# Performance work log

Hardware: AMD Instinct MI355X
Metric: run time of the kernel (lower is better)

The kernel has to match this reference:

```python
import jax, jax.numpy as jnp
import numpy as np

NQ = 4
PI_HALF = np.pi / 2
HAD = jnp.array([[1, 1], [1, -1]], dtype=jnp.complex64) / np.sqrt(2)
CNOT = jnp.array([[1, 0, 0, 0], [0, 1, 0, 0], [0, 0, 0, 1], [0, 0, 1, 0]], dtype=jnp.complex64)
_bits = (np.arange(2 ** NQ)[:, None] >> np.arange(NQ - 1, -1, -1)[None, :]) & 1
ZSIGNS = jnp.asarray(1.0 - 2.0 * _bits, jnp.float32)  # [16, NQ]


def _ry(theta):
    c = jnp.cos(theta / 2).astype(jnp.complex64)
    s = jnp.sin(theta / 2).astype(jnp.complex64)
    return jnp.stack([jnp.stack([c, -s], -1), jnp.stack([s, c], -1)], -2)  # [...,2,2]


def _rot(phi, theta, omega):
    # PennyLane Rot = RZ(omega) @ RY(theta) @ RZ(phi)
    c = jnp.cos(theta / 2).astype(jnp.complex64)
    s = jnp.sin(theta / 2).astype(jnp.complex64)
    ep = jnp.exp(0.5j * phi).astype(jnp.complex64)
    eo = jnp.exp(0.5j * omega).astype(jnp.complex64)
    return jnp.stack([jnp.stack([jnp.conj(ep) * jnp.conj(eo) * c, -ep * jnp.conj(eo) * s]),
                      jnp.stack([jnp.conj(ep) * eo * s, ep * eo * c])])


def _cry(theta):
    # controlled-RY, batched: [B] -> [B,4,4], basis order (control, target)
    B = theta.shape[0]
    U = jnp.zeros((B, 4, 4), jnp.complex64).at[:, 0, 0].set(1.0).at[:, 1, 1].set(1.0)
    return U.at[:, 2:, 2:].set(_ry(theta))


def _apply1(state, U, wire):
    s = jnp.moveaxis(state, wire + 1, 1)
    shp = s.shape
    s = s.reshape(shp[0], 2, -1)
    s = jnp.einsum('ij,bjk->bik', U, s) if U.ndim == 2 else jnp.einsum('bij,bjk->bik', U, s)
    return jnp.moveaxis(s.reshape(shp), 1, wire + 1)


def _apply2(state, U, q0, q1):
    s = jnp.moveaxis(state, (q0 + 1, q1 + 1), (1, 2))
    shp = s.shape
    s = s.reshape(shp[0], 4, -1)
    s = jnp.einsum('ij,bjk->bik', U, s) if U.ndim == 2 else jnp.einsum('bij,bjk->bik', U, s)
    return jnp.moveaxis(s.reshape(shp), (1, 2), (q0 + 1, q1 + 1))


def _init_state(B):
    s = jnp.zeros((B, 2 ** NQ), jnp.complex64).at[:, 0].set(1.0)
    return s.reshape((B,) + (2,) * NQ)


def _zexp(state):
    p = state.reshape(state.shape[0], -1)
    p = p.real ** 2 + p.imag ** 2
    return p @ ZSIGNS  # [B, NQ]


def _attention_circuit(q, k, params):
    # q, k: [E, NQ] angles; params: [NQ, 3] shared
    s = _init_state(q.shape[0])
    for i in range(NQ):
        s = _apply1(s, _ry(q[:, i]), i)
    for i in range(NQ):
        s = _apply1(s, HAD, i)
    for i in range(NQ):
        s = _apply2(s, _cry(k[:, i]), i, (i + 1) % NQ)
    for i in range(NQ):
        s = _apply1(s, _rot(params[i, 0], params[i, 1], params[i, 2]), i)
    return _zexp(s)


def _entangle_circuit(x, params):
    # x: [N, NQ] angles; params: [n_layers, NQ, 3]
    s = _init_state(x.shape[0])
    for i in range(NQ):
        s = _apply1(s, _ry(x[:, i]), i)
    for l in range(params.shape[0]):
        for i in range(NQ - 1):
            s = _apply2(s, CNOT, i, i + 1)
        for i in range(NQ):
            s = _apply1(s, _rot(params[l, i, 0], params[l, i, 1], params[l, i, 2]), i)
        s = _apply2(s, CNOT, 0, NQ - 1)  # n_qubits >= 4
    return _zexp(s)


def _path_circuit(x, params):
    # x: [N, NQ]; params: [3, NQ, 3]
    s = _init_state(x.shape[0])
    for i in range(NQ):
        s = _apply1(s, HAD, i)
    for i in range(NQ):
        s = _apply1(s, _ry(x[:, i]), i)
    for l in range(3):
        for i in range(NQ):
            s = _apply1(s, _rot(params[l, i, 0], params[l, i, 1], params[l, i, 2]), i)
        for i in range(NQ - 1):
            s = _apply2(s, CNOT, i, i + 1)
    return _zexp(s)


def _forward(x, W_in, b_in, lin_W, lin_b, qproj_W, qproj_b, ent_params,
             attq_W, attq_b, attk_W, attk_b, att_qp, path_params,
             path_in_W, path_in_b, path_out_W, path_out_b, out_W, out_b, edge_index):
    N = x.shape[0]
    loops = jnp.arange(N, dtype=edge_index.dtype)
    ei = jnp.concatenate([edge_index, jnp.stack([loops, loops])], axis=1)  # add_self_loops
    src, dst = ei[0], ei[1]
    h = jax.nn.relu(x @ W_in.T + b_in)
    for l in range(lin_W.shape[0]):
        x_cls = h @ lin_W[l].T + lin_b[l]
        xq = _entangle_circuit(jnp.tanh(h[:, :NQ]) * PI_HALF, ent_params[l])
        x_comb = x_cls + xq @ qproj_W[l].T + qproj_b[l]
        q = jnp.tanh(h @ attq_W[l].T + attq_b[l]) * PI_HALF
        k = jnp.tanh(h @ attk_W[l].T + attk_b[l]) * PI_HALF
        scores = _attention_circuit(q[src], k[dst], att_qp[l]).mean(axis=1)  # [E]
        att = jax.nn.softmax(scores)  # global softmax over all edges (faithful)
        h = jax.ops.segment_sum(att[:, None] * x_comb[src], dst, num_segments=N)
        h = jax.nn.relu(h)  # dropout is identity at eval
    pq = jnp.tanh(h @ path_in_W.T + path_in_b) * PI_HALF
    h = _path_circuit(pq, path_params) @ path_out_W.T + path_out_b
    return h @ out_W.T + out_b


def setup_inputs() -> dict:
    key = jax.random.key(0)
    ks = jax.random.split(key, 22)
    N, E, D_in, D_h, D_out, L = 20000, 300000, 64, 128, 32, 2
    w = lambda k, shape: jax.random.normal(k, shape, jnp.float32) * 0.1
    return {
        'x': jax.random.normal(ks[0], (N, D_in), jnp.float32),
        'W_in': w(ks[1], (D_h, D_in)), 'b_in': w(ks[2], (D_h,)),
        'lin_W': w(ks[3], (L, D_h, D_h)), 'lin_b': w(ks[4], (L, D_h)),
        'qproj_W': w(ks[5], (L, D_h, NQ)), 'qproj_b': w(ks[6], (L, D_h)),
        'ent_params': w(ks[7], (L, 2, NQ, 3)),
        'attq_W': w(ks[8], (L, NQ, D_h)), 'attq_b': w(ks[9], (L, NQ)),
        'attk_W': w(ks[10], (L, NQ, D_h)), 'attk_b': w(ks[11], (L, NQ)),
        'att_qp': w(ks[12], (L, NQ, 3)),
        'path_params': w(ks[13], (3, NQ, 3)),
        'path_in_W': w(ks[14], (NQ, D_h)), 'path_in_b': w(ks[15], (NQ,)),
        'path_out_W': w(ks[16], (D_h, NQ)), 'path_out_b': w(ks[17], (D_h,)),
        'out_W': w(ks[18], (D_out, D_h)), 'out_b': w(ks[19], (D_out,)),
        'edge_index': jax.random.randint(ks[20], (2, E), 0, N, dtype=jnp.int32),
    }


def reference(x, W_in, b_in, lin_W, lin_b, qproj_W, qproj_b, ent_params,
              attq_W, attq_b, attk_W, attk_b, att_qp, path_params,
              path_in_W, path_in_b, path_out_W, path_out_b, out_W, out_b, edge_index):
    return _forward(x, W_in, b_in, lin_W, lin_b, qproj_W, qproj_b, ent_params,
                    attq_W, attq_b, attk_W, attk_b, att_qp, path_params,
                    path_in_W, path_in_b, path_out_W, path_out_b, out_W, out_b, edge_index)
```

## Files before the change

### kernel.cpp

```cpp
#include <hip/hip_runtime.h>
#include <math.h>

#define PI_HALF 1.57079632679489662f

__device__ __forceinline__ float fast_tanh(float x) {
    float e = __expf(2.f * x);
    return 1.f - 2.f * __builtin_amdgcn_rcpf(e + 1.f);
}


__device__ __forceinline__ void prod_init(float sr[16],
        float c0, float s0, float c1, float s1,
        float c2, float s2, float c3, float s3) {
    float p2[4];
    p2[0] = c0 * c1; p2[1] = c0 * s1; p2[2] = s0 * c1; p2[3] = s0 * s1;
    float p3[8];
#pragma unroll
    for (int j = 0; j < 4; ++j) { p3[2 * j] = p2[j] * c2; p3[2 * j + 1] = p2[j] * s2; }
#pragma unroll
    for (int j = 0; j < 8; ++j) { sr[2 * j] = p3[j] * c3; sr[2 * j + 1] = p3[j] * s3; }
}

template<int M>
__device__ __forceinline__ void had_r(float sr[16]) {
    const float r = 0.70710678118654752f;
#pragma unroll
    for (int i = 0; i < 16; ++i) {
        if (i & M) continue;
        const int j = i | M;
        float ar = sr[i], br = sr[j];
        sr[i] = (ar + br) * r;
        sr[j] = (ar - br) * r;
    }
}

template<int MC, int MT>
__device__ __forceinline__ void cry_r(float sr[16], float c, float s) {
#pragma unroll
    for (int i = 0; i < 16; ++i) {
        if (!(i & MC) || (i & MT)) continue;
        const int j = i | MT;
        float ar = sr[i], br = sr[j];
        sr[i] = c * ar - s * br;
        sr[j] = s * ar + c * br;
    }
}

template<int MC, int MT>
__device__ __forceinline__ void cnot_r(float sr[16]) {
#pragma unroll
    for (int i = 0; i < 16; ++i) {
        if (!(i & MC) || (i & MT)) continue;
        const int j = i | MT;
        float t = sr[i]; sr[i] = sr[j]; sr[j] = t;
    }
}

template<int MC, int MT>
__device__ __forceinline__ void cnot_g(float sr[16], float si[16]) {
#pragma unroll
    for (int i = 0; i < 16; ++i) {
        if (!(i & MC) || (i & MT)) continue;
        const int j = i | MT;
        float tr = sr[i], ti = si[i];
        sr[i] = sr[j]; si[i] = si[j];
        sr[j] = tr;    si[j] = ti;
    }
}

template<int M>
__device__ __forceinline__ void rot_pre(float sr[16], float si[16], const float* __restrict__ u) {
    const float u00r = u[0], u00i = u[1], u01r = u[2], u01i = u[3];
    const float u10r = u[4], u10i = u[5], u11r = u[6], u11i = u[7];
#pragma unroll
    for (int i = 0; i < 16; ++i) {
        if (i & M) continue;
        const int j = i | M;
        float ar = sr[i], ai = si[i], br = sr[j], bi = si[j];
        sr[i] = u00r * ar - u00i * ai + u01r * br - u01i * bi;
        si[i] = u00r * ai + u00i * ar + u01r * bi + u01i * br;
        sr[j] = u10r * ar - u10i * ai + u11r * br - u11i * bi;
        si[j] = u10r * ai + u10i * ar + u11r * bi + u11i * br;
    }
}

template<int M>
__device__ __forceinline__ void rot_first(float sr[16], float si[16], const float* __restrict__ u) {
    const float u00r = u[0], u00i = u[1], u01r = u[2], u01i = u[3];
    const float u10r = u[4], u10i = u[5], u11r = u[6], u11i = u[7];
#pragma unroll
    for (int i = 0; i < 16; ++i) {
        if (i & M) continue;
        const int j = i | M;
        float ar = sr[i], br = sr[j];
        sr[i] = u00r * ar + u01r * br;
        si[i] = u00i * ar + u01i * br;
        sr[j] = u10r * ar + u11r * br;
        si[j] = u10i * ar + u11i * br;
    }
}

__device__ __forceinline__ void zexp_g(const float sr[16], const float si[16], float z[4]) {
    float p[16];
#pragma unroll
    for (int i = 0; i < 16; ++i) p[i] = sr[i] * sr[i] + si[i] * si[i];
    z[0] = z[1] = z[2] = z[3] = 0.f;
#pragma unroll
    for (int i = 0; i < 16; ++i) {
        z[0] += (i & 8) ? -p[i] : p[i];
        z[1] += (i & 4) ? -p[i] : p[i];
        z[2] += (i & 2) ? -p[i] : p[i];
        z[3] += (i & 1) ? -p[i] : p[i];
    }
}


__global__ void k_fsi(const float* __restrict__ entp, const float* __restrict__ attqp,
                      const float* __restrict__ pparm,
                      const float* __restrict__ outW, const float* __restrict__ outb,
                      const float* __restrict__ poW, const float* __restrict__ pob,
                      float* __restrict__ rotbuf, float* __restrict__ M,
                      float* __restrict__ v,
                      const float* __restrict__ x, const float* __restrict__ W,
                      const float* __restrict__ b, float* __restrict__ h,
                      int* __restrict__ cnt, float* __restrict__ sumexp, int N) {
    __shared__ float xs[32 * 64];
    const int bb = blockIdx.x;
    const int tid = threadIdx.x;
    {
        const int gid = bb * 256 + tid;
        const int T = gridDim.x * 256;
        for (int i = gid; i < N; i += T) cnt[i] = 0;
        if (gid < 4) sumexp[gid] = 0.f;
    }
    if (bb == 0) {
        const int t = tid;
        if (t < 36) {
            const float* p;
            if (t < 16)      p = entp  + t * 3;
            else if (t < 24) p = attqp + (t - 16) * 3;
            else             p = pparm + (t - 24) * 3;
            float phi = p[0], theta = p[1], omega = p[2];
            float st, ct; sincosf(0.5f * theta, &st, &ct);
            float sp, cp; sincosf(0.5f * (phi + omega), &sp, &cp);
            float sm, cm; sincosf(0.5f * (phi - omega), &sm, &cm);
            float* u = rotbuf + t * 8;
            u[0] =  ct * cp;  u[1] = -ct * sp;
            u[2] = -st * cm;  u[3] = -st * sm;
            u[4] =  st * cm;  u[5] = -st * sm;
            u[6] =  ct * cp;  u[7] =  ct * sp;
        } else if (t >= 64 && t < 192) {
            int t2 = t - 64;
            int o = t2 >> 2, i = t2 & 3;
            float acc = 0.f;
            for (int j = 0; j < 128; ++j) acc += outW[o * 128 + j] * poW[j * 4 + i];
            M[t2] = acc;
        } else if (t >= 192 && t < 224) {
            int o = t - 192;
            float acc = outb[o];
            for (int j = 0; j < 128; ++j) acc += outW[o * 128 + j] * pob[j];
            v[o] = acc;
        }
        return;
    }
    const int base = (bb - 1) * 32;
    for (int idx = tid; idx < 32 * 64; idx += 256) {
        int n = base + (idx >> 6);
        xs[idx] = (n < N) ? x[(size_t)n * 64 + (idx & 63)] : 0.f;
    }
    __syncthreads();
    const int lane = tid & 63;
    const int wv = tid >> 6;
    const int ch0 = lane, ch1 = lane + 64;
    float acc0[8], acc1[8];
#pragma unroll
    for (int n = 0; n < 8; ++n) { acc0[n] = 0.f; acc1[n] = 0.f; }
    const float4* w04 = (const float4*)(W + ch0 * 64);
    const float4* w14 = (const float4*)(W + ch1 * 64);
    for (int c4 = 0; c4 < 16; ++c4) {
        float4 wa = w04[c4];
        float4 wb = w14[c4];
#pragma unroll
        for (int n = 0; n < 8; ++n) {
            float4 hv = *(const float4*)&xs[(wv * 8 + n) * 64 + c4 * 4];
            acc0[n] += wa.x * hv.x + wa.y * hv.y + wa.z * hv.z + wa.w * hv.w;
            acc1[n] += wb.x * hv.x + wb.y * hv.y + wb.z * hv.z + wb.w * hv.w;
        }
    }
    const float b0 = b[ch0];
    const float b1 = b[ch1];
#pragma unroll
    for (int n = 0; n < 8; ++n) {
        int node = base + wv * 8 + n;
        if (node < N) {
            h[(size_t)node * 128 + ch0] = fmaxf(acc0[n] + b0, 0.f);
            h[(size_t)node * 128 + ch1] = fmaxf(acc1[n] + b1, 0.f);
        }
    }
}

__global__ void k_hist(const int* __restrict__ ei, int* __restrict__ cnt, int E, int EP) {
    int e = blockIdx.x * blockDim.x + threadIdx.x;
    if (e >= EP) return;
    int d_ = (e < E) ? ei[E + e] : e - E;
    atomicAdd(&cnt[d_], 1);
}

__global__ void k_scan(const int* __restrict__ cnt, int* __restrict__ off,
                       int* __restrict__ cur, int N) {
    __shared__ int tot[1024];
    const int t = threadIdx.x;
    const int chunk = (N + 1023) >> 10;
    const int s0 = t * chunk;
    const int s1 = min(s0 + chunk, N);
    int sum = 0;
    for (int i = s0; i < s1; ++i) sum += cnt[i];
    tot[t] = sum;
    __syncthreads();
    for (int d = 1; d < 1024; d <<= 1) {
        int v = (t >= d) ? tot[t - d] : 0;
        __syncthreads();
        tot[t] += v;
        __syncthreads();
    }
    int run = (t == 0) ? 0 : tot[t - 1];
    for (int i = s0; i < s1; ++i) {
        off[i] = run; cur[i] = run;
        run += cnt[i];
    }
}

#define HS_STRIDE 132
__global__ void k_entlin(const float* __restrict__ h, const float* __restrict__ rotE2,
                         const float* __restrict__ linW, const float* __restrict__ linb,
                         const float* __restrict__ qpW, const float* __restrict__ qpb,
                         const float* __restrict__ aqW, const float* __restrict__ aqb,
                         const float* __restrict__ akW, const float* __restrict__ akb,
                         float* __restrict__ xcomb, float* __restrict__ qbuf,
                         float* __restrict__ kbuf, int N,
                         const float* __restrict__ sprev,
                         int eblf, const int* __restrict__ ei,
                         int* __restrict__ cur, int* __restrict__ srcs,
                         int* __restrict__ inv, int E, int EP) {
    __shared__ float hs[16 * HS_STRIDE];
    __shared__ float xqs[16 * 4];
    const int tid = threadIdx.x;
    if (blockIdx.x < eblf) {
        int e = blockIdx.x * 128 + tid;
        if (e < EP) {
            int s_, d_;
            if (e < E) { s_ = ei[e]; d_ = ei[E + e]; } else { s_ = d_ = e - E; }
            int pos = atomicAdd(&cur[d_], 1);
            srcs[pos] = s_;
            inv[e] = pos;
        }
        return;
    }
    const int base = (blockIdx.x - eblf) * 16;
    const float scale = sprev ? __builtin_amdgcn_rcpf(sprev[0]) : 1.0f;
    for (int idx = tid; idx < 16 * 32; idx += 128) {
        int n = idx >> 5, c4 = idx & 31;
        int node = base + n;
        float4 hv = (node < N) ? *(const float4*)&h[(size_t)node * 128 + c4 * 4]
                               : make_float4(0.f, 0.f, 0.f, 0.f);
        hv.x *= scale; hv.y *= scale; hv.z *= scale; hv.w *= scale;
        *(float4*)&hs[n * HS_STRIDE + c4 * 4] = hv;
    }
    __syncthreads();
    if (tid < 64) {
#pragma unroll
        for (int rep = 0; rep < 2; ++rep) {
            const int dt = tid + rep * 64;
            const int nl = dt >> 3;
            const int which = dt & 7;
            const int qi = which & 3;
            const float4* Wp4 = (const float4*)(((which < 4) ? aqW : akW) + qi * 128);
            float dot = (which < 4) ? aqb[qi] : akb[qi];
            for (int c4 = 0; c4 < 32; ++c4) {
                float4 w = Wp4[c4];
                float4 hv = *(const float4*)&hs[nl * HS_STRIDE + c4 * 4];
                dot += w.x * hv.x + w.y * hv.y + w.z * hv.z + w.w * hv.w;
            }
            int node = base + nl;
            if (node < N) {
                float halfang = fast_tanh(dot) * (0.5f * PI_HALF);
                float s, c; __sincosf(halfang, &s, &c);
                float* dst = ((which < 4) ? qbuf : kbuf) + (size_t)node * 8 + qi * 2;
                dst[0] = c; dst[1] = s;
            }
        }
    } else if (tid < 80) {
        const int nl = tid - 64;
        if (base + nl < N) {
            float4 hv = *(const float4*)&hs[nl * HS_STRIDE];
            float c0, s0, c1, s1, c2, s2, c3, s3;
            { float a = fast_tanh(hv.x) * (0.5f * PI_HALF); __sincosf(a, &s0, &c0); }
            { float a = fast_tanh(hv.y) * (0.5f * PI_HALF); __sincosf(a, &s1, &c1); }
            { float a = fast_tanh(hv.z) * (0.5f * PI_HALF); __sincosf(a, &s2, &c2); }
            { float a = fast_tanh(hv.w) * (0.5f * PI_HALF); __sincosf(a, &s3, &c3); }
            float sr[16], si[16];
            prod_init(sr, c0, s0, c1, s1, c2, s2, c3, s3);
            cnot_r<8, 4>(sr); cnot_r<4, 2>(sr); cnot_r<2, 1>(sr);
            rot_first<8>(sr, si, rotE2);
            rot_pre<4>(sr, si, rotE2 + 8);
            rot_pre<2>(sr, si, rotE2 + 16);
            rot_pre<1>(sr, si, rotE2 + 24);
            cnot_g<8, 1>(sr, si);
            cnot_g<8, 4>(sr, si); cnot_g<4, 2>(sr, si); cnot_g<2, 1>(sr, si);
            const float* P = rotE2 + 32;
            rot_pre<8>(sr, si, P);
            rot_pre<4>(sr, si, P + 8);
            rot_pre<2>(sr, si, P + 16);
            rot_pre<1>(sr, si, P + 24);
            cnot_g<8, 1>(sr, si);
            float z[4]; zexp_g(sr, si, z);
            xqs[nl * 4 + 0] = z[0]; xqs[nl * 4 + 1] = z[1];
            xqs[nl * 4 + 2] = z[2]; xqs[nl * 4 + 3] = z[3];
        }
    }
    __syncthreads();
    const int lane = tid & 63;
    const int nh = tid >> 6;
    const int ch0 = lane, ch1 = lane + 64;
    float acc0[8], acc1[8];
#pragma unroll
    for (int n = 0; n < 8; ++n) { acc0[n] = 0.f; acc1[n] = 0.f; }
    const float4* w04 = (const float4*)(linW + ch0 * 128);
    const float4* w14 = (const float4*)(linW + ch1 * 128);
    for (int c4 = 0; c4 < 32; ++c4) {
        float4 wa = w04[c4];
        float4 wb = w14[c4];
#pragma unroll
        for (int n = 0; n < 8; ++n) {
            float4 hv = *(const float4*)&hs[(nh * 8 + n) * HS_STRIDE + c4 * 4];
            acc0[n] += wa.x * hv.x + wa.y * hv.y + wa.z * hv.z + wa.w * hv.w;
            acc1[n] += wb.x * hv.x + wb.y * hv.y + wb.z * hv.z + wb.w * hv.w;
        }
    }
    const float b0 = linb[ch0] + qpb[ch0];
    const float b1 = linb[ch1] + qpb[ch1];
    const float q00 = qpW[ch0 * 4 + 0], q01 = qpW[ch0 * 4 + 1];
    const float q02 = qpW[ch0 * 4 + 2], q03 = qpW[ch0 * 4 + 3];
    const float q10 = qpW[ch1 * 4 + 0], q11 = qpW[ch1 * 4 + 1];
    const float q12 = qpW[ch1 * 4 + 2], q13 = qpW[ch1 * 4 + 3];
#pragma unroll
    for (int n = 0; n < 8; ++n) {
        const int nl = nh * 8 + n;
        const int node = base + nl;
        if (node < N) {
            float x0 = xqs[nl * 4 + 0], x1 = xqs[nl * 4 + 1];
            float x2 = xqs[nl * 4 + 2], x3 = xqs[nl * 4 + 3];
            xcomb[(size_t)node * 128 + ch0] = acc0[n] + b0
                + q00 * x0 + q01 * x1 + q02 * x2 + q03 * x3;
            xcomb[(size_t)node * 128 + ch1] = acc1[n] + b1
                + q10 * x0 + q11 * x1 + q12 * x2 + q13 * x3;
        }
    }
}

__global__ void k_att(const float* __restrict__ qb, const float* __restrict__ kb,
                      const int* __restrict__ ei, const float* __restrict__ RA,
                      const int* __restrict__ inv, float* __restrict__ escore,
                      float* __restrict__ sumexp, int E, int EP) {
    __shared__ float red[4];
    int e = blockIdx.x * blockDim.x + threadIdx.x;
    float ex = 0.f;
    if (e < EP) {
        int s_, d_;
        if (e < E) { s_ = ei[e]; d_ = ei[E + e]; } else { s_ = d_ = e - E; }
        float4 qa = *(const float4*)&qb[(size_t)s_ * 8];
        float4 qc = *(const float4*)&qb[(size_t)s_ * 8 + 4];
        float4 ka = *(const float4*)&kb[(size_t)d_ * 8];
        float4 kc = *(const float4*)&kb[(size_t)d_ * 8 + 4];
        float sr[16], si[16];
        prod_init(sr, qa.x, qa.y, qa.z, qa.w, qc.x, qc.y, qc.z, qc.w);
        had_r<8>(sr); had_r<4>(sr); had_r<2>(sr); had_r<1>(sr);
        cry_r<8, 4>(sr, ka.x, ka.y);
        cry_r<4, 2>(sr, ka.z, ka.w);
        cry_r<2, 1>(sr, kc.x, kc.y);
        cry_r<1, 8>(sr, kc.z, kc.w);
        rot_first<8>(sr, si, RA);
        rot_pre<4>(sr, si, RA + 8);
        rot_pre<2>(sr, si, RA + 16);
        rot_pre<1>(sr, si, RA + 24);
        float p0  = sr[0]  * sr[0]  + si[0]  * si[0];
        float p1  = sr[1]  * sr[1]  + si[1]  * si[1];
        float p2  = sr[2]  * sr[2]  + si[2]  * si[2];
        float p4  = sr[4]  * sr[4]  + si[4]  * si[4];
        float p8  = sr[8]  * sr[8]  + si[8]  * si[8];
        float p7  = sr[7]  * sr[7]  + si[7]  * si[7];
        float p11 = sr[11] * sr[11] + si[11] * si[11];
        float p13 = sr[13] * sr[13] + si[13] * si[13];
        float p14 = sr[14] * sr[14] + si[14] * si[14];
        float p15 = sr[15] * sr[15] + si[15] * si[15];
        float sc = (p0 - p15) + 0.5f * ((p1 + p2 + p4 + p8) - (p7 + p11 + p13 + p14));
        ex = __expf(sc);
        escore[inv[e]] = ex;
    }
    float wsum = ex;
#pragma unroll
    for (int d = 32; d; d >>= 1) wsum += __shfl_xor(wsum, d, 64);
    if ((threadIdx.x & 63) == 0) red[threadIdx.x >> 6] = wsum;
    __syncthreads();
    if (threadIdx.x == 0) atomicAdd(sumexp, red[0] + red[1] + red[2] + red[3]);
}

__global__ void k_gather(const float* __restrict__ xcomb, const int* __restrict__ srcs,
                         const float* __restrict__ escore, const int* __restrict__ off,
                         const int* __restrict__ cnt, float* __restrict__ h) {
    __shared__ int sS[128];
    __shared__ float wS[128];
    const int b = blockIdx.x;
    const int tid = threadIdx.x;
    const int start = off[b];
    const int num = cnt[b];
    float acc = 0.f;
    for (int base = 0; base < num; base += 128) {
        int m = min(128, num - base);
        if (tid < m) {
            sS[tid] = srcs[start + base + tid];
            wS[tid] = escore[start + base + tid];
        }
        __syncthreads();
        int i = 0;
        for (; i + 8 <= m; i += 8) {
            float v0 = xcomb[(size_t)sS[i + 0] * 128 + tid];
            float v1 = xcomb[(size_t)sS[i + 1] * 128 + tid];
            float v2 = xcomb[(size_t)sS[i + 2] * 128 + tid];
            float v3 = xcomb[(size_t)sS[i + 3] * 128 + tid];
            float v4 = xcomb[(size_t)sS[i + 4] * 128 + tid];
            float v5 = xcomb[(size_t)sS[i + 5] * 128 + tid];
            float v6 = xcomb[(size_t)sS[i + 6] * 128 + tid];
            float v7 = xcomb[(size_t)sS[i + 7] * 128 + tid];
            acc += wS[i + 0] * v0; acc += wS[i + 1] * v1;
            acc += wS[i + 2] * v2; acc += wS[i + 3] * v3;
            acc += wS[i + 4] * v4; acc += wS[i + 5] * v5;
            acc += wS[i + 6] * v6; acc += wS[i + 7] * v7;
        }
        for (; i < m; ++i)
            acc += wS[i] * xcomb[(size_t)sS[i] * 128 + tid];
        __syncthreads();
    }
    h[(size_t)b * 128 + tid] = fmaxf(acc, 0.f);
}

__global__ void k_tail(const float* __restrict__ h, const float* __restrict__ piW,
                       const float* __restrict__ pib, const float* __restrict__ RP,
                       const float* __restrict__ M, const float* __restrict__ v,
                       const float* __restrict__ sprev,
                       float* __restrict__ out, int N) {
    __shared__ float pqS[64 * 8];
    __shared__ float zS[64 * 4];
    __shared__ float MS[128];
    __shared__ float vS[32];
    const int tid = threadIdx.x;
    const int base = blockIdx.x * 64;
    if (tid < 128) MS[tid] = M[tid];
    else if (tid < 160) vS[tid - 128] = v[tid - 128];
    const float invS = __builtin_amdgcn_rcpf(sprev[0]);
    {
        const int nl = tid >> 2, i = tid & 3;
        const int node = base + nl;
        if (node < N) {
            float raw = 0.f;
            const float4* w4 = (const float4*)(piW + i * 128);
            const float4* h4 = (const float4*)(h + (size_t)node * 128);
#pragma unroll 8
            for (int c4 = 0; c4 < 32; ++c4) {
                float4 w = w4[c4];
                float4 hv = h4[c4];
                raw += w.x * hv.x + w.y * hv.y + w.z * hv.z + w.w * hv.w;
            }
            float dot = pib[i] + invS * raw;
            float halfang = fast_tanh(dot) * (0.5f * PI_HALF);
            float s, c; __sincosf(halfang, &s, &c);
            pqS[nl * 8 + i * 2]     = c;
            pqS[nl * 8 + i * 2 + 1] = s;
        }
    }
    __syncthreads();
    if (tid < 64 && base + tid < N) {
        const float r = 0.70710678118654752f;
        float c0 = pqS[tid * 8 + 0], s0 = pqS[tid * 8 + 1];
        float c1 = pqS[tid * 8 + 2], s1 = pqS[tid * 8 + 3];
        float c2 = pqS[tid * 8 + 4], s2 = pqS[tid * 8 + 5];
        float c3 = pqS[tid * 8 + 6], s3 = pqS[tid * 8 + 7];
        float u0 = r * (c0 - s0), w0 = r * (c0 + s0);
        float u1 = r * (c1 - s1), w1 = r * (c1 + s1);
        float u2 = r * (c2 - s2), w2 = r * (c2 + s2);
        float u3 = r * (c3 - s3), w3 = r * (c3 + s3);
        float sr[16], si[16];
        prod_init(sr, u0, w0, u1, w1, u2, w2, u3, w3);
        rot_first<8>(sr, si, RP);
        rot_pre<4>(sr, si, RP + 8);
        rot_pre<2>(sr, si, RP + 16);
        rot_pre<1>(sr, si, RP + 24);
        cnot_g<8, 4>(sr, si); cnot_g<4, 2>(sr, si); cnot_g<2, 1>(sr, si);
#pragma unroll
        for (int l = 1; l < 3; ++l) {
            const float* P = RP + l * 32;
            rot_pre<8>(sr, si, P);
            rot_pre<4>(sr, si, P + 8);
            rot_pre<2>(sr, si, P + 16);
            rot_pre<1>(sr, si, P + 24);
            cnot_g<8, 4>(sr, si); cnot_g<4, 2>(sr, si); cnot_g<2, 1>(sr, si);
        }
        float z[4]; zexp_g(sr, si, z);
        zS[tid * 4 + 0] = z[0]; zS[tid * 4 + 1] = z[1];
        zS[tid * 4 + 2] = z[2]; zS[tid * 4 + 3] = z[3];
    }
    __syncthreads();
#pragma unroll
    for (int k = 0; k < 8; ++k) {
        int flat = k * 256 + tid;
        int nl = flat >> 5;
        int o = flat & 31;
        int node = base + nl;
        if (node < N) {
            out[(size_t)node * 32 + o] = vS[o]
                + MS[o * 4 + 0] * zS[nl * 4 + 0] + MS[o * 4 + 1] * zS[nl * 4 + 1]
                + MS[o * 4 + 2] * zS[nl * 4 + 2] + MS[o * 4 + 3] * zS[nl * 4 + 3];
        }
    }
}


extern "C" void kernel_launch(void* const* d_in, const int* in_sizes, int n_in,
                              void* d_out, int out_size, void* d_ws, size_t ws_size,
                              hipStream_t stream) {
    const float* x     = (const float*)d_in[0];
    const float* W_in  = (const float*)d_in[1];
    const float* b_in  = (const float*)d_in[2];
    const float* linW  = (const float*)d_in[3];
    const float* linb  = (const float*)d_in[4];
    const float* qpW   = (const float*)d_in[5];
    const float* qpb   = (const float*)d_in[6];
    const float* entp  = (const float*)d_in[7];
    const float* aqW   = (const float*)d_in[8];
    const float* aqb   = (const float*)d_in[9];
    const float* akW   = (const float*)d_in[10];
    const float* akb   = (const float*)d_in[11];
    const float* attqp = (const float*)d_in[12];
    const float* pparm = (const float*)d_in[13];
    const float* piW   = (const float*)d_in[14];
    const float* pib   = (const float*)d_in[15];
    const float* poW   = (const float*)d_in[16];
    const float* pob   = (const float*)d_in[17];
    const float* outW  = (const float*)d_in[18];
    const float* outb  = (const float*)d_in[19];
    const int*   ei    = (const int*)d_in[20];

    const int N  = in_sizes[0] / 64;
    const int E  = in_sizes[20] / 2;
    const int EP = E + N;

    float* ws     = (float*)d_ws;
    float* h      = ws;
    float* xcomb  = h      + (size_t)N * 128;
    float* qbuf   = xcomb  + (size_t)N * 128;
    float* kbuf   = qbuf   + (size_t)N * 8;
    float* escore = kbuf   + (size_t)N * 8;
    float* rotbuf = escore + EP;
    float* Mm     = rotbuf + 36 * 8;
    float* vv     = Mm + 128;
    int*   cnt    = (int*)(vv + 32);
    float* sumexp = (float*)(cnt + N);
    int*   off    = (int*)(sumexp + 4);
    int*   cur    = off + N;
    int*   srcs   = cur + N;
    int*   inv    = srcs + EP;

    const float* rotE = rotbuf;
    const float* rotA = rotbuf + 128;
    const float* rotP = rotbuf + 192;

    const int nb16 = (N + 15) / 16;
    const int nb32 = (N + 31) / 32;
    const int ebl  = (EP + 255) / 256;
    const int eblf = (EP + 127) / 128;

    k_fsi<<<nb32 + 1, 256, 0, stream>>>(entp, attqp, pparm, outW, outb, poW, pob,
                                        rotbuf, Mm, vv, x, W_in, b_in, h,
                                        cnt, sumexp, N);
    k_hist<<<ebl, 256, 0, stream>>>(ei, cnt, E, EP);
    k_scan<<<1, 1024, 0, stream>>>(cnt, off, cur, N);

    for (int l = 0; l < 2; ++l) {
        const int fillb = (l == 0) ? eblf : 0;
        k_entlin<<<fillb + nb16, 128, 0, stream>>>(h, rotE + l * 64,
            linW + (size_t)l * 128 * 128, linb + l * 128,
            qpW + (size_t)l * 128 * 4, qpb + l * 128,
            aqW + (size_t)l * 4 * 128, aqb + l * 4,
            akW + (size_t)l * 4 * 128, akb + l * 4,
            xcomb, qbuf, kbuf, N,
            (l == 0) ? (const float*)nullptr : (const float*)(sumexp + 0),
            fillb, ei, cur, srcs, inv, E, EP);
        k_att<<<ebl, 256, 0, stream>>>(qbuf, kbuf, ei, rotA + l * 32, inv,
                                       escore, sumexp + l, E, EP);
        k_gather<<<N, 128, 0, stream>>>(xcomb, srcs, escore, off, cnt, h);
    }

    k_tail<<<(N + 63) / 64, 256, 0, stream>>>(h, piW, pib, rotP, Mm, vv,
                                              sumexp + 1, (float*)d_out, N);
}
```

Before: 369.0 us.

## Split q/k and circuit work into own kernel; fuse linear with attention scoring

Moves the q/k angle dot products and the per-node entangling circuit out of the linear kernel into a separate, widely parallel kernel (one thread per node-output and per node), writing circuit expectations to a new xq buffer. The 128x128 linear layer is then co-launched in the same grid as the edge attention scoring, so the two independent workloads run concurrently instead of in separate launches. This removes serialized divergent sections inside the linear blocks, at the cost of an extra global round trip for xq and re-reading h from global memory for the dot products.

Result: no change. 361.8 us (-1.9%).

```diff
diff --git a/kernel.cpp b/kernel.cpp
--- a/kernel.cpp
+++ b/kernel.cpp
@@ -230,23 +230,20 @@
     }
 }
 
-#define HS_STRIDE 132
-__global__ void k_entlin(const float* __restrict__ h, const float* __restrict__ rotE2,
-                         const float* __restrict__ linW, const float* __restrict__ linb,
-                         const float* __restrict__ qpW, const float* __restrict__ qpb,
-                         const float* __restrict__ aqW, const float* __restrict__ aqb,
-                         const float* __restrict__ akW, const float* __restrict__ akb,
-                         float* __restrict__ xcomb, float* __restrict__ qbuf,
-                         float* __restrict__ kbuf, int N,
-                         const float* __restrict__ sprev,
-                         int eblf, const int* __restrict__ ei,
-                         int* __restrict__ cur, int* __restrict__ srcs,
-                         int* __restrict__ inv, int E, int EP) {
-    __shared__ float hs[16 * HS_STRIDE];
-    __shared__ float xqs[16 * 4];
+__global__ void k_qke(const float* __restrict__ h,
+                      const float* __restrict__ aqW, const float* __restrict__ aqb,
+                      const float* __restrict__ akW, const float* __restrict__ akb,
+                      const float* __restrict__ rotE2,
+                      float* __restrict__ qbuf, float* __restrict__ kbuf,
+                      float* __restrict__ xq, int N,
+                      const float* __restrict__ sprev,
+                      int fillb, int dotb, const int* __restrict__ ei,
+                      int* __restrict__ cur, int* __restrict__ srcs,
+                      int* __restrict__ inv, int E, int EP) {
+    int bb = blockIdx.x;
     const int tid = threadIdx.x;
-    if (blockIdx.x < eblf) {
-        int e = blockIdx.x * 128 + tid;
+    if (bb < fillb) {
+        int e = bb * 256 + tid;
         if (e < EP) {
             int s_, d_;
             if (e < E) { s_ = ei[e]; d_ = ei[E + e]; } else { s_ = d_ = e - E; }
@@ -256,7 +253,115 @@
         }
         return;
     }
-    const int base = (blockIdx.x - eblf) * 16;
+    bb -= fillb;
+    const float scale = sprev ? __builtin_amdgcn_rcpf(sprev[0]) : 1.0f;
+    if (bb < dotb) {
+        const int t = bb * 256 + tid;
+        const int node = t >> 3;
+        if (node >= N) return;
+        const int which = t & 7;
+        const int qi = which & 3;
+        const float4* h4 = (const float4*)(h + (size_t)node * 128);
+        const float4* w4 = (const float4*)(((which < 4) ? aqW : akW) + qi * 128);
+        float dot = (which < 4) ? aqb[qi] : akb[qi];
+        for (int c4 = 0; c4 < 32; ++c4) {
+            float4 hv = h4[c4];
+            hv.x *= scale; hv.y *= scale; hv.z *= scale; hv.w *= scale;
+            float4 w = w4[c4];
+            dot += w.x * hv.x + w.y * hv.y + w.z * hv.z + w.w * hv.w;
+        }
+        float halfang = fast_tanh(dot) * (0.5f * PI_HALF);
+        float s, c; __sincosf(halfang, &s, &c);
+        float* dst = ((which < 4) ? qbuf : kbuf) + (size_t)node * 8 + qi * 2;
+        dst[0] = c; dst[1] = s;
+        return;
+    }
+    bb -= dotb;
+    const int node = bb * 256 + tid;
+    if (node >= N) return;
+    float4 hv = *(const float4*)(h + (size_t)node * 128);
+    hv.x *= scale; hv.y *= scale; hv.z *= scale; hv.w *= scale;
+    float c0, s0, c1, s1, c2, s2, c3, s3;
+    { float a = fast_tanh(hv.x) * (0.5f * PI_HALF); __sincosf(a, &s0, &c0); }
+    { float a = fast_tanh(hv.y) * (0.5f * PI_HALF); __sincosf(a, &s1, &c1); }
+    { float a = fast_tanh(hv.z) * (0.5f * PI_HALF); __sincosf(a, &s2, &c2); }
+    { float a = fast_tanh(hv.w) * (0.5f * PI_HALF); __sincosf(a, &s3, &c3); }
+    float sr[16], si[16];
+    prod_init(sr, c0, s0, c1, s1, c2, s2, c3, s3);
+    cnot_r<8, 4>(sr); cnot_r<4, 2>(sr); cnot_r<2, 1>(sr);
+    rot_first<8>(sr, si, rotE2);
+    rot_pre<4>(sr, si, rotE2 + 8);
+    rot_pre<2>(sr, si, rotE2 + 16);
+    rot_pre<1>(sr, si, rotE2 + 24);
+    cnot_g<8, 1>(sr, si);
+    cnot_g<8, 4>(sr, si); cnot_g<4, 2>(sr, si); cnot_g<2, 1>(sr, si);
+    const float* P = rotE2 + 32;
+    rot_pre<8>(sr, si, P);
+    rot_pre<4>(sr, si, P + 8);
+    rot_pre<2>(sr, si, P + 16);
+    rot_pre<1>(sr, si, P + 24);
+    cnot_g<8, 1>(sr, si);
+    float z[4]; zexp_g(sr, si, z);
+    *(float4*)&xq[(size_t)node * 4] = make_float4(z[0], z[1], z[2], z[3]);
+}
+
+#define HS_STRIDE 132
+__global__ void k_linatt(const float* __restrict__ h, const float* __restrict__ xq,
+                         const float* __restrict__ linW, const float* __restrict__ linb,
+                         const float* __restrict__ qpW, const float* __restrict__ qpb,
+                         float* __restrict__ xcomb, int N,
+                         const float* __restrict__ sprev, int nb16,
+                         const float* __restrict__ qb, const float* __restrict__ kb,
+                         const int* __restrict__ ei, const float* __restrict__ RA,
+                         const int* __restrict__ inv, float* __restrict__ escore,
+                         float* __restrict__ sumexp, int E, int EP) {
+    __shared__ float hs[16 * HS_STRIDE];
+    __shared__ float red[2];
+    const int tid = threadIdx.x;
+    if (blockIdx.x >= nb16) {
+        int e = (blockIdx.x - nb16) * 128 + tid;
+        float ex = 0.f;
+        if (e < EP) {
+            int s_, d_;
+            if (e < E) { s_ = ei[e]; d_ = ei[E + e]; } else { s_ = d_ = e - E; }
+            float4 qa = *(const float4*)&qb[(size_t)s_ * 8];
+            float4 qc = *(const float4*)&qb[(size_t)s_ * 8 + 4];
+            float4 ka = *(const float4*)&kb[(size_t)d_ * 8];
+            float4 kc = *(const float4*)&kb[(size_t)d_ * 8 + 4];
+            float sr[16], si[16];
+            prod_init(sr, qa.x, qa.y, qa.z, qa.w, qc.x, qc.y, qc.z, qc.w);
+            had_r<8>(sr); had_r<4>(sr); had_r<2>(sr); had_r<1>(sr);
+            cry_r<8, 4>(sr, ka.x, ka.y);
+            cry_r<4, 2>(sr, ka.z, ka.w);
+            cry_r<2, 1>(sr, kc.x, kc.y);
+            cry_r<1, 8>(sr, kc.z, kc.w);
+            rot_first<8>(sr, si, RA);
+            rot_pre<4>(sr, si, RA + 8);
+            rot_pre<2>(sr, si, RA + 16);
+            rot_pre<1>(sr, si, RA + 24);
+            float p0  = sr[0]  * sr[0]  + si[0]  * si[0];
+            float p1  = sr[1]  * sr[1]  + si[1]  * si[1];
+            float p2  = sr[2]  * sr[2]  + si[2]  * si[2];
+            float p4  = sr[4]  * sr[4]  + si[4]  * si[4];
+            float p8  = sr[8]  * sr[8]  + si[8]  * si[8];
+            float p7  = sr[7]  * sr[7]  + si[7]  * si[7];
+            float p11 = sr[11] * sr[11] + si[11] * si[11];
+            float p13 = sr[13] * sr[13] + si[13] * si[13];
+            float p14 = sr[14] * sr[14] + si[14] * si[14];
+            float p15 = sr[15] * sr[15] + si[15] * si[15];
+            float sc = (p0 - p15) + 0.5f * ((p1 + p2 + p4 + p8) - (p7 + p11 + p13 + p14));
+            ex = __expf(sc);
+            escore[inv[e]] = ex;
+        }
+        float wsum = ex;
+#pragma unroll
+        for (int d = 32; d; d >>= 1) wsum += __shfl_xor(wsum, d, 64);
+        if ((tid & 63) == 0) red[tid >> 6] = wsum;
+        __syncthreads();
+        if (tid == 0) atomicAdd(sumexp, red[0] + red[1]);
+        return;
+    }
+    const int base = blockIdx.x * 16;
     const float scale = sprev ? __builtin_amdgcn_rcpf(sprev[0]) : 1.0f;
     for (int idx = tid; idx < 16 * 32; idx += 128) {
         int n = idx >> 5, c4 = idx & 31;
@@ -267,58 +372,6 @@
         *(float4*)&hs[n * HS_STRIDE + c4 * 4] = hv;
     }
     __syncthreads();
-    if (tid < 64) {
-#pragma unroll
-        for (int rep = 0; rep < 2; ++rep) {
-            const int dt = tid + rep * 64;
-            const int nl = dt >> 3;
-            const int which = dt & 7;
-            const int qi = which & 3;
-            const float4* Wp4 = (const float4*)(((which < 4) ? aqW : akW) + qi * 128);
-            float dot = (which < 4) ? aqb[qi] : akb[qi];
-            for (int c4 = 0; c4 < 32; ++c4) {
-                float4 w = Wp4[c4];
-                float4 hv = *(const float4*)&hs[nl * HS_STRIDE + c4 * 4];
-                dot += w.x * hv.x + w.y * hv.y + w.z * hv.z + w.w * hv.w;
-            }
-            int node = base + nl;
-            if (node < N) {
-                float halfang = fast_tanh(dot) * (0.5f * PI_HALF);
-                float s, c; __sincosf(halfang, &s, &c);
-                float* dst = ((which < 4) ? qbuf : kbuf) + (size_t)node * 8 + qi * 2;
-                dst[0] = c; dst[1] = s;
-            }
-        }
-    } else if (tid < 80) {
-        const int nl = tid - 64;
-        if (base + nl < N) {
-            float4 hv = *(const float4*)&hs[nl * HS_STRIDE];
-            float c0, s0, c1, s1, c2, s2, c3, s3;
-            { float a = fast_tanh(hv.x) * (0.5f * PI_HALF); __sincosf(a, &s0, &c0); }
-            { float a = fast_tanh(hv.y) * (0.5f * PI_HALF); __sincosf(a, &s1, &c1); }
-            { float a = fast_tanh(hv.z) * (0.5f * PI_HALF); __sincosf(a, &s2, &c2); }
-            { float a = fast_tanh(hv.w) * (0.5f * PI_HALF); __sincosf(a, &s3, &c3); }
-            float sr[16], si[16];
-            prod_init(sr, c0, s0, c1, s1, c2, s2, c3, s3);
-            cnot_r<8, 4>(sr); cnot_r<4, 2>(sr); cnot_r<2, 1>(sr);
-            rot_first<8>(sr, si, rotE2);
-            rot_pre<4>(sr, si, rotE2 + 8);
-            rot_pre<2>(sr, si, rotE2 + 16);
-            rot_pre<1>(sr, si, rotE2 + 24);
-            cnot_g<8, 1>(sr, si);
-            cnot_g<8, 4>(sr, si); cnot_g<4, 2>(sr, si); cnot_g<2, 1>(sr, si);
-            const float* P = rotE2 + 32;
-            rot_pre<8>(sr, si, P);
-            rot_pre<4>(sr, si, P + 8);
-            rot_pre<2>(sr, si, P + 16);
-            rot_pre<1>(sr, si, P + 24);
-            cnot_g<8, 1>(sr, si);
-            float z[4]; zexp_g(sr, si, z);
-            xqs[nl * 4 + 0] = z[0]; xqs[nl * 4 + 1] = z[1];
-            xqs[nl * 4 + 2] = z[2]; xqs[nl * 4 + 3] = z[3];
-        }
-    }
-    __syncthreads();
     const int lane = tid & 63;
     const int nh = tid >> 6;
     const int ch0 = lane, ch1 = lane + 64;
@@ -348,61 +401,13 @@
         const int nl = nh * 8 + n;
         const int node = base + nl;
         if (node < N) {
-            float x0 = xqs[nl * 4 + 0], x1 = xqs[nl * 4 + 1];
-            float x2 = xqs[nl * 4 + 2], x3 = xqs[nl * 4 + 3];
+            float4 xv = *(const float4*)&xq[(size_t)node * 4];
             xcomb[(size_t)node * 128 + ch0] = acc0[n] + b0
-                + q00 * x0 + q01 * x1 + q02 * x2 + q03 * x3;
+                + q00 * xv.x + q01 * xv.y + q02 * xv.z + q03 * xv.w;
             xcomb[(size_t)node * 128 + ch1] = acc1[n] + b1
-                + q10 * x0 + q11 * x1 + q12 * x2 + q13 * x3;
-        }
-    }
-}
-
-__global__ void k_att(const float* __restrict__ qb, const float* __restrict__ kb,
-                      const int* __restrict__ ei, const float* __restrict__ RA,
-                      const int* __restrict__ inv, float* __restrict__ escore,
-                      float* __restrict__ sumexp, int E, int EP) {
-    __shared__ float red[4];
-    int e = blockIdx.x * blockDim.x + threadIdx.x;
-    float ex = 0.f;
-    if (e < EP) {
-        int s_, d_;
-        if (e < E) { s_ = ei[e]; d_ = ei[E + e]; } else { s_ = d_ = e - E; }
-        float4 qa = *(const float4*)&qb[(size_t)s_ * 8];
-        float4 qc = *(const float4*)&qb[(size_t)s_ * 8 + 4];
-        float4 ka = *(const float4*)&kb[(size_t)d_ * 8];
-        float4 kc = *(const float4*)&kb[(size_t)d_ * 8 + 4];
-        float sr[16], si[16];
-        prod_init(sr, qa.x, qa.y, qa.z, qa.w, qc.x, qc.y, qc.z, qc.w);
-        had_r<8>(sr); had_r<4>(sr); had_r<2>(sr); had_r<1>(sr);
-        cry_r<8, 4>(sr, ka.x, ka.y);
-        cry_r<4, 2>(sr, ka.z, ka.w);
-        cry_r<2, 1>(sr, kc.x, kc.y);
-        cry_r<1, 8>(sr, kc.z, kc.w);
-        rot_first<8>(sr, si, RA);
-        rot_pre<4>(sr, si, RA + 8);
-        rot_pre<2>(sr, si, RA + 16);
-        rot_pre<1>(sr, si, RA + 24);
-        float p0  = sr[0]  * sr[0]  + si[0]  * si[0];
-        float p1  = sr[1]  * sr[1]  + si[1]  * si[1];
-        float p2  = sr[2]  * sr[2]  + si[2]  * si[2];
-        float p4  = sr[4]  * sr[4]  + si[4]  * si[4];
-        float p8  = sr[8]  * sr[8]  + si[8]  * si[8];
-        float p7  = sr[7]  * sr[7]  + si[7]  * si[7];
-        float p11 = sr[11] * sr[11] + si[11] * si[11];
-        float p13 = sr[13] * sr[13] + si[13] * si[13];
-        float p14 = sr[14] * sr[14] + si[14] * si[14];
-        float p15 = sr[15] * sr[15] + si[15] * si[15];
-        float sc = (p0 - p15) + 0.5f * ((p1 + p2 + p4 + p8) - (p7 + p11 + p13 + p14));
-        ex = __expf(sc);
-        escore[inv[e]] = ex;
-    }
-    float wsum = ex;
-#pragma unroll
-    for (int d = 32; d; d >>= 1) wsum += __shfl_xor(wsum, d, 64);
-    if ((threadIdx.x & 63) == 0) red[threadIdx.x >> 6] = wsum;
-    __syncthreads();
-    if (threadIdx.x == 0) atomicAdd(sumexp, red[0] + red[1] + red[2] + red[3]);
+                + q10 * xv.x + q11 * xv.y + q12 * xv.z + q13 * xv.w;
+        }
+    }
 }
 
 __global__ void k_gather(const float* __restrict__ xcomb, const int* __restrict__ srcs,
@@ -569,6 +574,7 @@
     int*   cur    = off + N;
     int*   srcs   = cur + N;
     int*   inv    = srcs + EP;
+    float* xq     = (float*)(inv + EP);
 
     const float* rotE = rotbuf;
     const float* rotA = rotbuf + 128;
@@ -577,7 +583,9 @@
     const int nb16 = (N + 15) / 16;
     const int nb32 = (N + 31) / 32;
     const int ebl  = (EP + 255) / 256;
-    const int eblf = (EP + 127) / 128;
+    const int ebl128 = (EP + 127) / 128;
+    const int dotb = (N * 8 + 255) / 256;
+    const int circb = (N + 255) / 256;
 
     k_fsi<<<nb32 + 1, 256, 0, stream>>>(entp, attqp, pparm, outW, outb, poW, pob,
                                         rotbuf, Mm, vv, x, W_in, b_in, h,
@@ -586,17 +594,19 @@
     k_scan<<<1, 1024, 0, stream>>>(cnt, off, cur, N);
 
     for (int l = 0; l < 2; ++l) {
-        const int fillb = (l == 0) ? eblf : 0;
-        k_entlin<<<fillb + nb16, 128, 0, stream>>>(h, rotE + l * 64,
+        const int fillb = (l == 0) ? ebl : 0;
+        const float* sprev = (l == 0) ? (const float*)nullptr
+                                      : (const float*)(sumexp + 0);
+        k_qke<<<fillb + dotb + circb, 256, 0, stream>>>(h,
+            aqW + (size_t)l * 4 * 128, aqb + l * 4,
+            akW + (size_t)l * 4 * 128, akb + l * 4,
+            rotE + l * 64, qbuf, kbuf, xq, N, sprev,
+            fillb, dotb, ei, cur, srcs, inv, E, EP);
+        k_linatt<<<nb16 + ebl128, 128, 0, stream>>>(h, xq,
             linW + (size_t)l * 128 * 128, linb + l * 128,
             qpW + (size_t)l * 128 * 4, qpb + l * 128,
-            aqW + (size_t)l * 4 * 128, aqb + l * 4,
-            akW + (size_t)l * 4 * 128, akb + l * 4,
-            xcomb, qbuf, kbuf, N,
-            (l == 0) ? (const float*)nullptr : (const float*)(sumexp + 0),
-            fillb, ei, cur, srcs, inv, E, EP);
-        k_att<<<ebl, 256, 0, stream>>>(qbuf, kbuf, ei, rotA + l * 32, inv,
-                                       escore, sumexp + l, E, EP);
+            xcomb, N, sprev, nb16,
+            qbuf, kbuf, ei, rotA + l * 32, inv, escore, sumexp + l, E, EP);
         k_gather<<<N, 128, 0, stream>>>(xcomb, srcs, escore, off, cnt, h);
     }
 
```
